# Performance work log

Measured on AMD Instinct MI355X. Metric: run time of the kernel, lower is better.

The kernel has to match this reference:

```python
import jax, jax.numpy as jnp
import numpy as np

B, N, E = 64, 256, 512   # batch, leaves (power of 2), embed_size
D, U = 512, 512          # tree_size, units (controller size == units)


def setup_inputs() -> dict:
    key = jax.random.key(0)
    ks = jax.random.split(key, 11)
    sc = lambda k, shape: jax.random.normal(k, shape, dtype=jnp.float32) * 0.05
    return {
        "inputs": jax.random.normal(ks[0], (B, N, E), dtype=jnp.float32),
        "h0": sc(ks[1], (B, U)),
        "c0": sc(ks[2], (B, U)),
        "W_t": sc(ks[3], (E, D)),          # Transformer
        "W_j": sc(ks[4], (2 * D, D)),      # Join
        "W_s": sc(ks[5], (D + U, 1)),      # Search
        "W_h": sc(ks[6], (D + U, D)),      # Write candidate
        "W_T": sc(ks[7], (D + U, 1)),      # Write gate
        "kernel": sc(ks[8], (E, 4 * U)),   # LSTM input kernel (i,f,c,o)
        "rec_kernel": sc(ks[9], (U, 4 * U)),
        "bias": jnp.zeros((4 * U,), jnp.float32),
    }


def reference(inputs, h0, c0, W_t, W_j, W_s, W_h, W_T, kernel, rec_kernel, bias):
    b, n, e = inputs.shape
    control = h0  # control = previous LSTM hidden state

    # --- leaf embed: Transformer, batched over all leaves ---
    leaf_h = jax.nn.relu(jnp.einsum('bne,ed->bnd', inputs, W_t))  # [B,N,D]

    # --- refresh: bottom-up join, batched per tree level ---
    levels = [leaf_h]
    h = leaf_h
    while h.shape[1] > 1:
        pair = jnp.concatenate([h[:, 0::2], h[:, 1::2]], axis=-1)  # [B,m/2,2D]
        h = jax.nn.relu(jnp.einsum('bmk,kd->bmd', pair, W_j))
        levels.append(h)

    # --- retrieve: top-down search producing leaf attentions ---
    # Searches all use refresh-time h (parent search happens before any
    # update in its subtree), so a level-batched top-down pass is exact.
    attn = jnp.ones((b, 1, 1), inputs.dtype)
    for lvl in range(len(levels) - 1, 0, -1):
        node_h = levels[lvl]                     # [B,m,D]
        m = node_h.shape[1]
        ctrl = jnp.broadcast_to(control[:, None, :], (b, m, control.shape[-1]))
        mr = jax.nn.sigmoid(jnp.einsum('bmk,ko->bmo',
                                       jnp.concatenate([node_h, ctrl], -1), W_s))  # [B,m,1]
        # children interleave: left gets attn*(1-mr), right gets attn*mr
        attn = jnp.concatenate([attn * (1.0 - mr), attn * mr], axis=-1).reshape(b, 2 * m, 1)

    tree_out = jnp.sum(attn * inputs, axis=1)  # [B,E] soft-retrieved leaf value

    # --- write update of leaf memories, batched over all leaves ---
    ctrl = jnp.broadcast_to(control[:, None, :], (b, n, control.shape[-1]))
    data = jnp.concatenate([leaf_h, ctrl], -1)                     # [B,N,D+U]
    cand = jax.nn.sigmoid(jnp.einsum('bnk,kd->bnd', data, W_h))
    upd = jax.nn.sigmoid(jnp.einsum('bnk,ko->bno', data, W_T))
    written = upd * cand + (1.0 - upd) * leaf_h
    leaf_h_new = attn * written + (1.0 - attn) * leaf_h            # [B,N,D]

    # --- LSTM cell update (keras LSTMCell gate order i,f,c,o) ---
    z = tree_out @ kernel + h0 @ rec_kernel + bias
    zi, zf, zg, zo = jnp.split(z, 4, axis=-1)
    c_new = jax.nn.sigmoid(zf) * c0 + jax.nn.sigmoid(zi) * jnp.tanh(zg)
    h_new = jax.nn.sigmoid(zo) * jnp.tanh(c_new)
    return h_new, c_new, leaf_h_new
```

## Files before the change

### kernel.cpp

```cpp
#include <hip/hip_runtime.h>
#include <hip/hip_bf16.h>
#include <cstdint>
#include <cstddef>


__device__ __forceinline__ float sigmoidf_(float x) { return 1.0f / (1.0f + __expf(-x)); }

typedef __attribute__((ext_vector_type(8))) short bf16x8;
typedef __attribute__((ext_vector_type(4))) float f32x4;

__device__ __forceinline__ void load_lds16(const void* g, void* l) {
  __builtin_amdgcn_global_load_lds((const __attribute__((address_space(1))) void*)g,
                                   (__attribute__((address_space(3))) void*)l, 16, 0, 0);
}

__global__ __launch_bounds__(256)
void tconv_all(const float* __restrict__ W_t, const float* __restrict__ W_j,
               const float* __restrict__ W_h,
               __hip_bfloat16* __restrict__ Wt_t, __hip_bfloat16* __restrict__ Wt_j,
               __hip_bfloat16* __restrict__ Wt_h) {
  const int z = blockIdx.z;
  if (z != 1 && blockIdx.x >= 16) return;
  const int K = (z == 1) ? 1024 : 512;
  const float* W = (z == 0) ? W_t : ((z == 1) ? W_j : W_h);
  __hip_bfloat16* Wt = (z == 0) ? Wt_t : ((z == 1) ? Wt_j : Wt_h);
  __shared__ float sh[32][33];
  const int tx = threadIdx.x & 31, ty = threadIdx.x >> 5;
  const int k0 = blockIdx.x * 32, n0 = blockIdx.y * 32;
#pragma unroll
  for (int i = 0; i < 4; ++i)
    sh[ty + i * 8][tx] = W[(size_t)(k0 + ty + i * 8) * 512 + n0 + tx];
  __syncthreads();
#pragma unroll
  for (int i = 0; i < 4; ++i)
    Wt[(size_t)(n0 + ty + i * 8) * K + k0 + tx] = __float2bfloat16(sh[tx][ty + i * 8]);
}

template<int MODE, bool AFP32>
__global__ __launch_bounds__(256)
void mfma_gemm(const __hip_bfloat16* __restrict__ A, const float* __restrict__ Af,
               const __hip_bfloat16* __restrict__ Bt, int M, int K,
               __hip_bfloat16* __restrict__ Cb, float* __restrict__ Cf,
               const float* __restrict__ ctrl_h, const float* __restrict__ attn,
               const float* __restrict__ upd, const __hip_bfloat16* __restrict__ leaf) {
  __shared__ __align__(16) __hip_bfloat16 Asm[128 * 32];
  __shared__ __align__(16) __hip_bfloat16 Bsm[128 * 32];
  const int tid = threadIdx.x;
  const int wave = tid >> 6, lane = tid & 63;
  const int bm = blockIdx.y * 128, bn = blockIdx.x * 128;
  const int wm = (wave >> 1) * 64, wn = (wave & 1) * 64;
  const int q = lane >> 4, lr = lane & 15;

  f32x4 acc[4][4] = {};

  const int c0 = wave * 128 + lane, c1 = c0 + 64;
  const size_t ga0 = (size_t)(bm + (c0 >> 2)) * K + (c0 & 3) * 8;
  const size_t ga1 = (size_t)(bm + (c1 >> 2)) * K + (c1 & 3) * 8;
  const size_t gb0 = (size_t)(bn + (c0 >> 2)) * K + (c0 & 3) * 8;
  const size_t gb1 = (size_t)(bn + (c1 >> 2)) * K + (c1 & 3) * 8;
  __hip_bfloat16* la0 = Asm + wave * 1024;
  __hip_bfloat16* la1 = Asm + wave * 1024 + 512;
  __hip_bfloat16* lb0 = Bsm + wave * 1024;
  __hip_bfloat16* lb1 = Bsm + wave * 1024 + 512;

  for (int k0v = 0; k0v < K; k0v += 32) {
    if (AFP32) {
#pragma unroll
      for (int it = 0; it < 4; ++it) {
        const int c = it * 256 + tid;
        const int row = c >> 3, kc = c & 7;
        float4 v = *(const float4*)(Af + (size_t)(bm + row) * K + k0v + kc * 4);
        __hip_bfloat16 h[4] = {__float2bfloat16(v.x), __float2bfloat16(v.y),
                               __float2bfloat16(v.z), __float2bfloat16(v.w)};
        *(ushort4*)(Asm + row * 32 + kc * 4) = *(ushort4*)h;
      }
    } else {
      load_lds16(A + ga0 + k0v, la0);
      load_lds16(A + ga1 + k0v, la1);
    }
    load_lds16(Bt + gb0 + k0v, lb0);
    load_lds16(Bt + gb1 + k0v, lb1);
    __syncthreads();
    bf16x8 af[4], bfr[4];
#pragma unroll
    for (int mt = 0; mt < 4; ++mt)
      af[mt] = *(const bf16x8*)(Asm + (wm + mt * 16 + lr) * 32 + q * 8);
#pragma unroll
    for (int nt = 0; nt < 4; ++nt)
      bfr[nt] = *(const bf16x8*)(Bsm + (wn + nt * 16 + lr) * 32 + q * 8);
#pragma unroll
    for (int mt = 0; mt < 4; ++mt)
#pragma unroll
      for (int nt = 0; nt < 4; ++nt)
        acc[mt][nt] = __builtin_amdgcn_mfma_f32_16x16x32_bf16(af[mt], bfr[nt], acc[mt][nt], 0, 0, 0);
    __syncthreads();
  }

  if (MODE == 0) {
#pragma unroll
    for (int mt = 0; mt < 4; ++mt) {
      const int rbase = bm + wm + mt * 16 + q * 4;
#pragma unroll
      for (int nt = 0; nt < 4; ++nt) {
        const int col = bn + wn + nt * 16 + lr;
#pragma unroll
        for (int r = 0; r < 4; ++r) {
          const int row = rbase + r;
          if (row < M)
            Cb[(size_t)row * 512 + col] = __float2bfloat16(fmaxf(acc[mt][nt][r], 0.f));
        }
      }
    }
  } else {
#pragma unroll
    for (int mt = 0; mt < 4; ++mt) {
      const int rbase = bm + wm + mt * 16 + q * 4;
#pragma unroll
      for (int r = 0; r < 4; ++r) {
        const int row = rbase + r;
        const float a = attn[row];
        const float u = upd[row];
        const int bidx = row >> 8;
#pragma unroll
        for (int nt = 0; nt < 4; ++nt) {
          const int col = bn + wn + nt * 16 + lr;
          const float cand = sigmoidf_(acc[mt][nt][r] + ctrl_h[(size_t)bidx * 512 + col]);
          const float lf = __bfloat162float(leaf[(size_t)row * 512 + col]);
          const float w = u * cand + (1.f - u) * lf;
          Cf[(size_t)row * 512 + col] = a * w + (1.f - a) * lf;
        }
      }
    }
  }
}

__global__ __launch_bounds__(256)
void join_level(const __hip_bfloat16* __restrict__ in, __hip_bfloat16* __restrict__ outp,
                const __hip_bfloat16* __restrict__ Wt_j) {
  const int wave = threadIdx.x >> 6, lane = threadIdx.x & 63;
  const int q = lane >> 4, lr = lane & 15;
  const int tile = blockIdx.x * 4 + wave;
  const int mtile = tile >> 5, ntile = tile & 31;
  const __hip_bfloat16* ap = in + (size_t)(mtile * 16 + lr) * 1024 + q * 8;
  const __hip_bfloat16* bp = Wt_j + (size_t)(ntile * 16 + lr) * 1024 + q * 8;
  f32x4 acc = {0.f, 0.f, 0.f, 0.f};
#pragma unroll 8
  for (int k0 = 0; k0 < 1024; k0 += 32) {
    bf16x8 a  = *(const bf16x8*)(ap + k0);
    bf16x8 bb = *(const bf16x8*)(bp + k0);
    acc = __builtin_amdgcn_mfma_f32_16x16x32_bf16(a, bb, acc, 0, 0, 0);
  }
  const int col = ntile * 16 + lr;
  const int orow = mtile * 16 + q * 4;
#pragma unroll
  for (int r = 0; r < 4; ++r)
    outp[(size_t)(orow + r) * 512 + col] = __float2bfloat16(fmaxf(acc[r], 0.f));
}

__global__ __launch_bounds__(256)
void gemv_dual(const __hip_bfloat16* __restrict__ leaf,
               const __hip_bfloat16* __restrict__ levels,
               const float* __restrict__ W_T, const float* __restrict__ W_s,
               const float* __restrict__ ctrlT,
               float* __restrict__ upd, float* __restrict__ sc) {
  const int wave = threadIdx.x >> 6, lane = threadIdx.x & 63;
  const int bid = blockIdx.x;
  const bool is_upd = bid < 4096;
  const int row = (is_upd ? bid : (bid - 4096)) * 4 + wave;
  const __hip_bfloat16* X = is_upd ? leaf : levels;
  const float* w = is_upd ? W_T : W_s;
  union { bf16x8 v; __hip_bfloat16 e[8]; } u;
  u.v = *(const bf16x8*)(X + (size_t)row * 512 + lane * 8);
  const float* wp = w + lane * 8;
  float p = 0.f;
#pragma unroll
  for (int j = 0; j < 8; ++j) p += __bfloat162float(u.e[j]) * wp[j];
#pragma unroll
  for (int off = 32; off > 0; off >>= 1) p += __shfl_down(p, off);
  if (lane == 0) {
    if (is_upd) upd[row] = sigmoidf_(p + ctrlT[row >> 8]);
    else        sc[row] = p;
  }
}

__global__ __launch_bounds__(256)
void prep_ctrl(const float* __restrict__ h0, const float* __restrict__ W_T,
               float* __restrict__ ctrlT) {
  const int b = blockIdx.x, tid = threadIdx.x;
  __shared__ float part[256];
  float p = 0.f;
  for (int i = tid; i < 512; i += 256) p += h0[b * 512 + i] * W_T[512 + i];
  part[tid] = p; __syncthreads();
  for (int s = 128; s > 0; s >>= 1) { if (tid < s) part[tid] += part[tid + s]; __syncthreads(); }
  if (tid == 0) ctrlT[b] = part[0];
}

__global__ __launch_bounds__(256)
void propagate(const float* __restrict__ sc, const float* __restrict__ h0,
               const float* __restrict__ W_s, float* __restrict__ attn_out) {
  const int b = blockIdx.x, tid = threadIdx.x;
  __shared__ float part[256], attn_sh[256], newattn[256];
  __shared__ float scs;
  float p = 0.f;
  for (int i = tid; i < 512; i += 256) p += h0[b * 512 + i] * W_s[512 + i];
  part[tid] = p; __syncthreads();
  for (int s = 128; s > 0; s >>= 1) { if (tid < s) part[tid] += part[tid + s]; __syncthreads(); }
  if (tid == 0) { scs = part[0]; attn_sh[0] = 1.f; }
  __syncthreads();
  const int row_off[9] = {0, 0, 8192, 12288, 14336, 15360, 15872, 16128, 16256};
#pragma unroll
  for (int l = 8; l >= 1; --l) {
    const int m = 256 >> l;
    if (tid < m) {
      const float mr = sigmoidf_(sc[row_off[l] + b * m + tid] + scs);
      const float a = attn_sh[tid];
      newattn[2 * tid]     = a * (1.f - mr);
      newattn[2 * tid + 1] = a * mr;
    }
    __syncthreads();
    if (tid < 2 * m) attn_sh[tid] = newattn[tid];
    __syncthreads();
  }
  attn_out[b * 256 + tid] = attn_sh[tid];
}

__global__ __launch_bounds__(256)
void tree_part(const float* __restrict__ inputs, const float* __restrict__ attn,
               float* __restrict__ tp) {
  const int s = blockIdx.x, b = blockIdx.y;
  const int tid = threadIdx.x;
  __shared__ float a_sh[64];
  if (tid < 64) a_sh[tid] = attn[b * 256 + s * 64 + tid];
  __syncthreads();
  float acc0 = 0.f, acc1 = 0.f;
  const float* base = inputs + ((size_t)b * 256 + s * 64) * 512;
  for (int nn = 0; nn < 64; ++nn) {
    const float a = a_sh[nn];
    const float* row = base + (size_t)nn * 512;
    acc0 += a * row[tid];
    acc1 += a * row[tid + 256];
  }
  tp[((size_t)s * 64 + b) * 512 + tid]       = acc0;
  tp[((size_t)s * 64 + b) * 512 + tid + 256] = acc1;
}

__global__ __launch_bounds__(256)
void tree_reduce(const float* __restrict__ tp, float* __restrict__ tre) {
  const int i = blockIdx.x * 256 + threadIdx.x;
  tre[i] = tp[i] + tp[32768 + i] + tp[65536 + i] + tp[98304 + i];
}

__global__ __launch_bounds__(256)
void ctrl_gemm(const float* __restrict__ h0, const float* __restrict__ W_h,
               float* __restrict__ chp) {
  const int col = blockIdx.x * 256 + threadIdx.x;
  const int b   = blockIdx.y;
  const int z   = blockIdx.z;
  __shared__ float hsh[128];
  if (threadIdx.x < 128) hsh[threadIdx.x] = h0[b * 512 + z * 128 + threadIdx.x];
  __syncthreads();
  const float* Wp = W_h + (size_t)(512 + z * 128) * 512 + col;
  float s = 0.f;
#pragma unroll 8
  for (int k = 0; k < 128; ++k) s += hsh[k] * Wp[(size_t)k * 512];
  chp[((size_t)z * 64 + b) * 512 + col] = s;
}

__global__ __launch_bounds__(256)
void ctrl_reduce(const float* __restrict__ chp, float* __restrict__ ch) {
  const int i = blockIdx.x * 256 + threadIdx.x;
  ch[i] = chp[i] + chp[32768 + i] + chp[65536 + i] + chp[98304 + i];
}

__global__ __launch_bounds__(256)
void lstm_gemm_splitk(const float* __restrict__ tre, const float* __restrict__ h0,
                      const float* __restrict__ kern, const float* __restrict__ rec,
                      float* __restrict__ Zp) {
  const int tid = threadIdx.x;
  const int col = blockIdx.x * 256 + tid;
  const int b0 = blockIdx.y * 4;
  const int z = blockIdx.z;
  const float* X = (z < 4) ? tre : h0;
  const float* W = (z < 4) ? (kern + (size_t)z * 128 * 2048)
                           : (rec + (size_t)(z - 4) * 128 * 2048);
  const int koff = (z & 3) * 128;
  __shared__ float xs[4][128];
  for (int i = tid; i < 512; i += 256) {
    int bb = i >> 7, k = i & 127;
    xs[bb][k] = X[(b0 + bb) * 512 + koff + k];
  }
  __syncthreads();
  float a0 = 0.f, a1 = 0.f, a2 = 0.f, a3 = 0.f;
#pragma unroll 8
  for (int k = 0; k < 128; ++k) {
    const float w = W[(size_t)k * 2048 + col];
    a0 += xs[0][k] * w;
    a1 += xs[1][k] * w;
    a2 += xs[2][k] * w;
    a3 += xs[3][k] * w;
  }
  Zp[((size_t)z * 64 + b0 + 0) * 2048 + col] = a0;
  Zp[((size_t)z * 64 + b0 + 1) * 2048 + col] = a1;
  Zp[((size_t)z * 64 + b0 + 2) * 2048 + col] = a2;
  Zp[((size_t)z * 64 + b0 + 3) * 2048 + col] = a3;
}

__global__ __launch_bounds__(256)
void lstm_combine(const float* __restrict__ Zp, const float* __restrict__ bias,
                  const float* __restrict__ c0,
                  float* __restrict__ out_h, float* __restrict__ out_c) {
  const int i = blockIdx.x * 256 + threadIdx.x;
  const int b = i >> 9, u = i & 511;
  float zi = bias[u], zf = bias[512 + u], zg = bias[1024 + u], zo = bias[1536 + u];
#pragma unroll
  for (int z = 0; z < 8; ++z) {
    const size_t base = ((size_t)z * 64 + b) * 2048;
    zi += Zp[base + u];
    zf += Zp[base + 512 + u];
    zg += Zp[base + 1024 + u];
    zo += Zp[base + 1536 + u];
  }
  const float c = sigmoidf_(zf) * c0[i] + sigmoidf_(zi) * tanhf(zg);
  out_h[i] = sigmoidf_(zo) * tanhf(c);
  out_c[i] = c;
}

extern "C" void kernel_launch(void* const* d_in, const int* in_sizes, int n_in,
                              void* d_out, int out_size, void* d_ws, size_t ws_size,
                              hipStream_t stream) {
  const float* inputs = (const float*)d_in[0];
  const float* h0     = (const float*)d_in[1];
  const float* c0     = (const float*)d_in[2];
  const float* W_t    = (const float*)d_in[3];
  const float* W_j    = (const float*)d_in[4];
  const float* W_s    = (const float*)d_in[5];
  const float* W_h    = (const float*)d_in[6];
  const float* W_T    = (const float*)d_in[7];
  const float* kern   = (const float*)d_in[8];
  const float* rec    = (const float*)d_in[9];
  const float* bias   = (const float*)d_in[10];
  float* out = (float*)d_out;

  char* p = (char*)d_ws;
  __hip_bfloat16* leaf_bf   = (__hip_bfloat16*)p; p += 16777216;
  __hip_bfloat16* levels_bf = (__hip_bfloat16*)p; p += 16842752;
  __hip_bfloat16* Wt_t      = (__hip_bfloat16*)p; p += 524288;
  __hip_bfloat16* Wt_j      = (__hip_bfloat16*)p; p += 1048576;
  __hip_bfloat16* Wt_h      = (__hip_bfloat16*)p; p += 524288;
  float* attn  = (float*)p; p += 65536;
  float* upd   = (float*)p; p += 65536;
  float* tre   = (float*)p; p += 131072;
  float* chp   = (float*)p; p += 524288;
  float* ch    = (float*)p; p += 131072;
  float* Zp    = (float*)p; p += 4194304;
  float* sc    = (float*)p; p += 65536;
  float* ctrlT = (float*)p; p += 4096;
  float* tp    = (float*)p; p += 524288;

  tconv_all<<<dim3(32, 16, 3), 256, 0, stream>>>(W_t, W_j, W_h, Wt_t, Wt_j, Wt_h);
  ctrl_gemm<<<dim3(2, 64, 4), 256, 0, stream>>>(h0, W_h, chp);
  ctrl_reduce<<<128, 256, 0, stream>>>(chp, ch);
  prep_ctrl<<<64, 256, 0, stream>>>(h0, W_T, ctrlT);

  mfma_gemm<0, true><<<dim3(4, 128), 256, 0, stream>>>(
      nullptr, inputs, Wt_t, 16384, 512,
      leaf_bf, nullptr, nullptr, nullptr, nullptr, nullptr);

  const int lvl_off_h[9] = {0, 0, 4194304, 6291456, 7340032,
                            7864320, 8126464, 8257536, 8323072};
  const __hip_bfloat16* Aptr = leaf_bf;
  for (int l = 1; l <= 3; ++l) {
    const int M = 64 * (256 >> l);
    __hip_bfloat16* Cl = levels_bf + lvl_off_h[l];
    mfma_gemm<0, false><<<dim3(4, M / 128), 256, 0, stream>>>(
        Aptr, nullptr, Wt_j, M, 1024,
        Cl, nullptr, nullptr, nullptr, nullptr, nullptr);
    Aptr = Cl;
  }
  for (int l = 4; l <= 8; ++l) {
    const int m_out = 256 >> l;
    join_level<<<32 * m_out, 256, 0, stream>>>(levels_bf + lvl_off_h[l - 1],
                                               levels_bf + lvl_off_h[l], Wt_j);
  }

  gemv_dual<<<8176, 256, 0, stream>>>(leaf_bf, levels_bf, W_T, W_s, ctrlT, upd, sc);
  propagate<<<64, 256, 0, stream>>>(sc, h0, W_s, attn);

  tree_part<<<dim3(4, 64), 256, 0, stream>>>(inputs, attn, tp);
  tree_reduce<<<128, 256, 0, stream>>>(tp, tre);

  mfma_gemm<1, false><<<dim3(4, 128), 256, 0, stream>>>(
      leaf_bf, nullptr, Wt_h, 16384, 512,
      nullptr, out + 65536, ch, attn, upd, leaf_bf);
  lstm_gemm_splitk<<<dim3(8, 16, 8), 256, 0, stream>>>(tre, h0, kern, rec, Zp);
  lstm_combine<<<128, 256, 0, stream>>>(Zp, bias, c0, out, out + 32768);
}
```

Baseline: 334.2 us.

## Pre-convert inputs to bf16, swap GEMM grid order, fuse small reduction kernels

Adds a separate kernel that converts the fp32 inputs to bf16, so the leaf-embed GEMM takes the bf16 path; it falls back to the fp32 path when the workspace is too small. Swaps the blockIdx x/y roles in the MFMA GEMM so consecutive blocks walk along M, which changes L2 reuse of the weight tiles. Replaces the split-K control GEMM and its reduce kernel with one full-K kernel, and folds the tree partial-sum reduction into the LSTM GEMM input load, removing two launches. The tradeoff is an extra 32MB read plus a 16MB write for the conversion, and a longer serial K loop in the control GEMM.

```diff
diff --git a/kernel.cpp b/kernel.cpp
--- a/kernel.cpp
+++ b/kernel.cpp
@@ -12,6 +12,19 @@
 __device__ __forceinline__ void load_lds16(const void* g, void* l) {
   __builtin_amdgcn_global_load_lds((const __attribute__((address_space(1))) void*)g,
                                    (__attribute__((address_space(3))) void*)l, 16, 0, 0);
+}
+
+__global__ __launch_bounds__(256)
+void cvt_inputs(const float* __restrict__ in, __hip_bfloat16* __restrict__ outp) {
+  const size_t i = ((size_t)blockIdx.x * 256 + threadIdx.x) * 8;
+  float4 v0 = *(const float4*)(in + i);
+  float4 v1 = *(const float4*)(in + i + 4);
+  union { __hip_bfloat16 h[8]; bf16x8 v; } u;
+  u.h[0] = __float2bfloat16(v0.x); u.h[1] = __float2bfloat16(v0.y);
+  u.h[2] = __float2bfloat16(v0.z); u.h[3] = __float2bfloat16(v0.w);
+  u.h[4] = __float2bfloat16(v1.x); u.h[5] = __float2bfloat16(v1.y);
+  u.h[6] = __float2bfloat16(v1.z); u.h[7] = __float2bfloat16(v1.w);
+  *(bf16x8*)(outp + i) = u.v;
 }
 
 __global__ __launch_bounds__(256)
@@ -47,7 +60,7 @@
   __shared__ __align__(16) __hip_bfloat16 Bsm[128 * 32];
   const int tid = threadIdx.x;
   const int wave = tid >> 6, lane = tid & 63;
-  const int bm = blockIdx.y * 128, bn = blockIdx.x * 128;
+  const int bm = blockIdx.x * 128, bn = blockIdx.y * 128;
   const int wm = (wave >> 1) * 64, wn = (wave & 1) * 64;
   const int q = lane >> 4, lr = lane & 15;
 
@@ -245,49 +258,40 @@
 }
 
 __global__ __launch_bounds__(256)
-void tree_reduce(const float* __restrict__ tp, float* __restrict__ tre) {
-  const int i = blockIdx.x * 256 + threadIdx.x;
-  tre[i] = tp[i] + tp[32768 + i] + tp[65536 + i] + tp[98304 + i];
-}
-
-__global__ __launch_bounds__(256)
-void ctrl_gemm(const float* __restrict__ h0, const float* __restrict__ W_h,
-               float* __restrict__ chp) {
+void ctrl_full(const float* __restrict__ h0, const float* __restrict__ W_h,
+               float* __restrict__ ch) {
+  const int b = blockIdx.y;
   const int col = blockIdx.x * 256 + threadIdx.x;
-  const int b   = blockIdx.y;
-  const int z   = blockIdx.z;
-  __shared__ float hsh[128];
-  if (threadIdx.x < 128) hsh[threadIdx.x] = h0[b * 512 + z * 128 + threadIdx.x];
+  __shared__ float hsh[512];
+  hsh[threadIdx.x]       = h0[b * 512 + threadIdx.x];
+  hsh[threadIdx.x + 256] = h0[b * 512 + 256 + threadIdx.x];
   __syncthreads();
-  const float* Wp = W_h + (size_t)(512 + z * 128) * 512 + col;
+  const float* Wp = W_h + (size_t)512 * 512 + col;
   float s = 0.f;
 #pragma unroll 8
-  for (int k = 0; k < 128; ++k) s += hsh[k] * Wp[(size_t)k * 512];
-  chp[((size_t)z * 64 + b) * 512 + col] = s;
-}
-
-__global__ __launch_bounds__(256)
-void ctrl_reduce(const float* __restrict__ chp, float* __restrict__ ch) {
-  const int i = blockIdx.x * 256 + threadIdx.x;
-  ch[i] = chp[i] + chp[32768 + i] + chp[65536 + i] + chp[98304 + i];
-}
-
-__global__ __launch_bounds__(256)
-void lstm_gemm_splitk(const float* __restrict__ tre, const float* __restrict__ h0,
+  for (int k = 0; k < 512; ++k) s += hsh[k] * Wp[(size_t)k * 512];
+  ch[(size_t)b * 512 + col] = s;
+}
+
+__global__ __launch_bounds__(256)
+void lstm_gemm_splitk(const float* __restrict__ tp, const float* __restrict__ h0,
                       const float* __restrict__ kern, const float* __restrict__ rec,
                       float* __restrict__ Zp) {
   const int tid = threadIdx.x;
   const int col = blockIdx.x * 256 + tid;
   const int b0 = blockIdx.y * 4;
   const int z = blockIdx.z;
-  const float* X = (z < 4) ? tre : h0;
   const float* W = (z < 4) ? (kern + (size_t)z * 128 * 2048)
                            : (rec + (size_t)(z - 4) * 128 * 2048);
   const int koff = (z & 3) * 128;
   __shared__ float xs[4][128];
   for (int i = tid; i < 512; i += 256) {
     int bb = i >> 7, k = i & 127;
-    xs[bb][k] = X[(b0 + bb) * 512 + koff + k];
+    const size_t idx = (size_t)(b0 + bb) * 512 + koff + k;
+    float x;
+    if (z < 4) x = tp[idx] + tp[32768 + idx] + tp[65536 + idx] + tp[98304 + idx];
+    else       x = h0[idx];
+    xs[bb][k] = x;
   }
   __syncthreads();
   float a0 = 0.f, a1 = 0.f, a2 = 0.f, a3 = 0.f;
@@ -349,22 +353,28 @@
   __hip_bfloat16* Wt_h      = (__hip_bfloat16*)p; p += 524288;
   float* attn  = (float*)p; p += 65536;
   float* upd   = (float*)p; p += 65536;
-  float* tre   = (float*)p; p += 131072;
-  float* chp   = (float*)p; p += 524288;
   float* ch    = (float*)p; p += 131072;
   float* Zp    = (float*)p; p += 4194304;
   float* sc    = (float*)p; p += 65536;
   float* ctrlT = (float*)p; p += 4096;
   float* tp    = (float*)p; p += 524288;
+  const bool use_cvt = ws_size >= (size_t)(p - (char*)d_ws) + 16777216;
+  __hip_bfloat16* inputs_bf = (__hip_bfloat16*)p;
 
   tconv_all<<<dim3(32, 16, 3), 256, 0, stream>>>(W_t, W_j, W_h, Wt_t, Wt_j, Wt_h);
-  ctrl_gemm<<<dim3(2, 64, 4), 256, 0, stream>>>(h0, W_h, chp);
-  ctrl_reduce<<<128, 256, 0, stream>>>(chp, ch);
+  ctrl_full<<<dim3(2, 64), 256, 0, stream>>>(h0, W_h, ch);
   prep_ctrl<<<64, 256, 0, stream>>>(h0, W_T, ctrlT);
 
-  mfma_gemm<0, true><<<dim3(4, 128), 256, 0, stream>>>(
-      nullptr, inputs, Wt_t, 16384, 512,
-      leaf_bf, nullptr, nullptr, nullptr, nullptr, nullptr);
+  if (use_cvt) {
+    cvt_inputs<<<4096, 256, 0, stream>>>(inputs, inputs_bf);
+    mfma_gemm<0, false><<<dim3(128, 4), 256, 0, stream>>>(
+        inputs_bf, nullptr, Wt_t, 16384, 512,
+        leaf_bf, nullptr, nullptr, nullptr, nullptr, nullptr);
+  } else {
+    mfma_gemm<0, true><<<dim3(128, 4), 256, 0, stream>>>(
+        nullptr, inputs, Wt_t, 16384, 512,
+        leaf_bf, nullptr, nullptr, nullptr, nullptr, nullptr);
+  }
 
   const int lvl_off_h[9] = {0, 0, 4194304, 6291456, 7340032,
                             7864320, 8126464, 8257536, 8323072};
@@ -372,7 +382,7 @@
   for (int l = 1; l <= 3; ++l) {
     const int M = 64 * (256 >> l);
     __hip_bfloat16* Cl = levels_bf + lvl_off_h[l];
-    mfma_gemm<0, false><<<dim3(4, M / 128), 256, 0, stream>>>(
+    mfma_gemm<0, false><<<dim3(M / 128, 4), 256, 0, stream>>>(
         Aptr, nullptr, Wt_j, M, 1024,
         Cl, nullptr, nullptr, nullptr, nullptr, nullptr);
     Aptr = Cl;
@@ -387,11 +397,10 @@
   propagate<<<64, 256, 0, stream>>>(sc, h0, W_s, attn);
 
   tree_part<<<dim3(4, 64), 256, 0, stream>>>(inputs, attn, tp);
-  tree_reduce<<<128, 256, 0, stream>>>(tp, tre);
-
-  mfma_gemm<1, false><<<dim3(4, 128), 256, 0, stream>>>(
+
+  mfma_gemm<1, false><<<dim3(128, 4), 256, 0, stream>>>(
       leaf_bf, nullptr, Wt_h, 16384, 512,
       nullptr, out + 65536, ch, attn, upd, leaf_bf);
-  lstm_gemm_splitk<<<dim3(8, 16, 8), 256, 0, stream>>>(tre, h0, kern, rec, Zp);
+  lstm_gemm_splitk<<<dim3(8, 16, 8), 256, 0, stream>>>(tp, h0, kern, rec, Zp);
   lstm_combine<<<128, 256, 0, stream>>>(Zp, bias, c0, out, out + 32768);
 }
```

New measurement: 336.3 us. About the same (+0.7%).
